# Performance work log

Measured on AMD Instinct MI355X. Metric: run time of the kernel, lower is better.

Reference implementation:

```python
import jax, jax.numpy as jnp
import numpy as np

N_NODES = 100000
N_EDGES = 1600000
IN_C, HID_C, OUT_C = 128, 256, 256


def sage_conv(x, src, dst, W_l, b_l, W_r, n_nodes):
    # mean aggregation of source-node features onto destination nodes
    msg_sum = jax.ops.segment_sum(x[src], dst, num_segments=n_nodes)  # [N, F]
    deg = jax.ops.segment_sum(jnp.ones_like(dst, dtype=x.dtype), dst, num_segments=n_nodes)
    aggr = msg_sum / jnp.maximum(deg, 1.0)[:, None]
    # PyG SAGEConv: lin_l(aggr) (with bias) + lin_r(x) (no bias)
    return aggr @ W_l + b_l + x @ W_r


def setup_inputs() -> dict:
    key = jax.random.key(0)
    ks = jax.random.split(key, 12)
    x = jax.random.normal(ks[0], (N_NODES, IN_C), dtype=jnp.float32)
    edge_src = jax.random.randint(ks[1], (N_EDGES,), 0, N_NODES)
    edge_dst = jax.random.randint(ks[2], (N_EDGES,), 0, N_NODES)

    def glorot(k, fan_in, fan_out):
        s = jnp.sqrt(2.0 / (fan_in + fan_out)).astype(jnp.float32)
        return jax.random.normal(k, (fan_in, fan_out), dtype=jnp.float32) * s

    return {
        "x": x,
        "W_l0": glorot(ks[3], IN_C, HID_C), "b_l0": jnp.zeros((HID_C,), jnp.float32),
        "W_r0": glorot(ks[4], IN_C, HID_C),
        "W_l1": glorot(ks[5], HID_C, HID_C), "b_l1": jnp.zeros((HID_C,), jnp.float32),
        "W_r1": glorot(ks[6], HID_C, HID_C),
        "W_l2": glorot(ks[7], HID_C, OUT_C), "b_l2": jnp.zeros((OUT_C,), jnp.float32),
        "W_r2": glorot(ks[8], HID_C, OUT_C),
        "edge_src": edge_src,
        "edge_dst": edge_dst,
    }


def reference(x, W_l0, b_l0, W_r0, W_l1, b_l1, W_r1, W_l2, b_l2, W_r2, edge_src, edge_dst):
    n = x.shape[0]
    h = sage_conv(x, edge_src, edge_dst, W_l0, b_l0, W_r0, n)
    h = jax.nn.relu(h)  # dropout p=0.0 -> identity
    h = sage_conv(h, edge_src, edge_dst, W_l1, b_l1, W_r1, n)
    h = jax.nn.relu(h)
    h = sage_conv(h, edge_src, edge_dst, W_l2, b_l2, W_r2, n)
    return h
```

## Files before the change

kernel.cpp:

```cpp
#include <hip/hip_runtime.h>
#include <cstdint>
#include <cstddef>


#define N_NODES 100000
#define N_EDGES 1600000

#define SCAN_BLOCKS 256
#define SCAN_T 256
#define FILL_PASSES 4

typedef unsigned short ushort;
typedef unsigned int uint;
typedef __attribute__((ext_vector_type(8))) short short8;
typedef __attribute__((ext_vector_type(4))) float floatx4;

#define AS1 __attribute__((address_space(1)))
#define AS3 __attribute__((address_space(3)))

__device__ __forceinline__ float bf2f(ushort h) {
    union { uint u; float f; } c; c.u = ((uint)h) << 16; return c.f;
}
__device__ __forceinline__ ushort f2bf(float f) {
    union { float f; uint u; } c; c.f = f;
    uint u = c.u;
    return (ushort)((u + 0x7FFFu + ((u >> 16) & 1u)) >> 16);
}


#define N4X (N_NODES * 128 / 4)

__global__ void prep_all(
    const int* __restrict__ dst, int* __restrict__ cnt,
    const float* __restrict__ x, ushort* __restrict__ xb,
    const float* __restrict__ Wl0, ushort* __restrict__ Wl0t,
    const float* __restrict__ Wr0, ushort* __restrict__ Wr0t,
    const float* __restrict__ Wl1, ushort* __restrict__ Wl1t,
    const float* __restrict__ Wr1, ushort* __restrict__ Wr1t,
    const float* __restrict__ Wl2, ushort* __restrict__ Wl2t,
    const float* __restrict__ Wr2, ushort* __restrict__ Wr2t)
{
    int i = blockIdx.x * blockDim.x + threadIdx.x;
    if (i < N_EDGES) { atomicAdd(&cnt[dst[i]], 1); return; }
    i -= N_EDGES;
    if (i < N4X) {
        float4 v = *(const float4*)&x[(size_t)i * 4];
        ushort4 o;
        o.x = f2bf(v.x); o.y = f2bf(v.y); o.z = f2bf(v.z); o.w = f2bf(v.w);
        *(ushort4*)&xb[(size_t)i * 4] = o;
        return;
    }
    i -= N4X;
#define WT2(Wsrc, Wdst, LIM) \
    if (i < (LIM)) { \
        int q = i >> 11, col = (i >> 3) & 255, e = i & 7; \
        Wdst[i] = f2bf(Wsrc[(q * 8 + e) * 256 + col]); \
        return; \
    } \
    i -= (LIM);
    WT2(Wl0, Wl0t, 32768)
    WT2(Wr0, Wr0t, 32768)
    WT2(Wl1, Wl1t, 65536)
    WT2(Wr1, Wr1t, 65536)
    WT2(Wl2, Wl2t, 65536)
    WT2(Wr2, Wr2t, 65536)
#undef WT2
}


__global__ __launch_bounds__(SCAN_T) void scan_partial(
    const int* __restrict__ cnt, int* __restrict__ bsum, int n)
{
    int chunk = (n + SCAN_BLOCKS - 1) / SCAN_BLOCKS;
    int beg = blockIdx.x * chunk;
    int end = beg + chunk; if (end > n) end = n;
    int t = threadIdx.x;
    int s = 0;
    for (int i = beg + t; i < end; i += SCAN_T) s += cnt[i];
    __shared__ int sh[SCAN_T];
    sh[t] = s;
    __syncthreads();
    for (int off = SCAN_T / 2; off > 0; off >>= 1) {
        if (t < off) sh[t] += sh[t + off];
        __syncthreads();
    }
    if (t == 0) bsum[blockIdx.x] = sh[0];
}

__global__ __launch_bounds__(SCAN_T) void scan_block_sums(int* __restrict__ bsum) {
    int t = threadIdx.x;
    __shared__ int sh[SCAN_T];
    int v = bsum[t];
    sh[t] = v;
    __syncthreads();
    for (int off = 1; off < SCAN_T; off <<= 1) {
        int u = (t >= off) ? sh[t - off] : 0;
        __syncthreads();
        sh[t] += u;
        __syncthreads();
    }
    bsum[t] = sh[t] - v;
}

__global__ __launch_bounds__(SCAN_T) void scan_fill(
    int* __restrict__ cnt, const int* __restrict__ bsum,
    int* __restrict__ row_ptr, int n)
{
    int chunk = (n + SCAN_BLOCKS - 1) / SCAN_BLOCKS;
    int beg = blockIdx.x * chunk;
    int end = beg + chunk; if (end > n) end = n;
    int t = threadIdx.x;
    int per = (chunk + SCAN_T - 1) / SCAN_T;
    int tb = beg + t * per;
    int te = tb + per; if (te > end) te = end;
    int s = 0;
    for (int i = tb; i < te; ++i) s += cnt[i];
    __shared__ int sh[SCAN_T];
    sh[t] = s;
    __syncthreads();
    for (int off = 1; off < SCAN_T; off <<= 1) {
        int u = (t >= off) ? sh[t - off] : 0;
        __syncthreads();
        sh[t] += u;
        __syncthreads();
    }
    int running = bsum[blockIdx.x] + sh[t] - s;
    for (int i = tb; i < te; ++i) {
        int c = cnt[i];
        row_ptr[i] = running;
        cnt[i] = running;
        running += c;
    }
    if (blockIdx.x == 0 && t == 0) row_ptr[n] = N_EDGES;
}

__global__ void fill_csr(const int* __restrict__ src, const int* __restrict__ dst,
                         int* __restrict__ cursor, int* __restrict__ col_idx) {
    int i = blockIdx.x * blockDim.x + threadIdx.x;
    if (i >= N_EDGES) return;
    int lo = (int)blockIdx.y * (N_NODES / FILL_PASSES);
    int hi = lo + (N_NODES / FILL_PASSES);
    int d = dst[i];
    if (d >= lo && d < hi) {
        int p = atomicAdd(&cursor[d], 1);
        col_idx[p] = src[i];
    }
}

__global__ __launch_bounds__(64) void aggregate_bf16(
    const ushort* __restrict__ xb, const int* __restrict__ row_ptr,
    const int* __restrict__ col_idx, ushort* __restrict__ outb, int F)
{
    int node = blockIdx.x;
    int t = threadIdx.x;
    int b = row_ptr[node], e = row_ptr[node + 1];
    float d = (float)(e - b); if (d < 1.f) d = 1.f;
    float inv = 1.f / d;

    if (F == 256) {
        int c = t * 4;
        float a0 = 0.f, a1 = 0.f, a2 = 0.f, a3 = 0.f;
        float b0 = 0.f, b1 = 0.f, b2 = 0.f, b3 = 0.f;
        int i = b;
        for (; i + 1 < e; i += 2) {
            int s0 = col_idx[i];
            int s1 = col_idx[i + 1];
            uint2 v0 = *(const uint2*)&xb[(size_t)s0 * 256 + c];
            uint2 v1 = *(const uint2*)&xb[(size_t)s1 * 256 + c];
            a0 += bf2f((ushort)(v0.x & 0xffff)); a1 += bf2f((ushort)(v0.x >> 16));
            a2 += bf2f((ushort)(v0.y & 0xffff)); a3 += bf2f((ushort)(v0.y >> 16));
            b0 += bf2f((ushort)(v1.x & 0xffff)); b1 += bf2f((ushort)(v1.x >> 16));
            b2 += bf2f((ushort)(v1.y & 0xffff)); b3 += bf2f((ushort)(v1.y >> 16));
        }
        if (i < e) {
            int s0 = col_idx[i];
            uint2 v0 = *(const uint2*)&xb[(size_t)s0 * 256 + c];
            a0 += bf2f((ushort)(v0.x & 0xffff)); a1 += bf2f((ushort)(v0.x >> 16));
            a2 += bf2f((ushort)(v0.y & 0xffff)); a3 += bf2f((ushort)(v0.y >> 16));
        }
        ushort4 o;
        o.x = f2bf((a0 + b0) * inv); o.y = f2bf((a1 + b1) * inv);
        o.z = f2bf((a2 + b2) * inv); o.w = f2bf((a3 + b3) * inv);
        *(ushort4*)&outb[(size_t)node * 256 + c] = o;
    } else {
        int c = t * 2;
        float a0 = 0.f, a1 = 0.f, b0 = 0.f, b1 = 0.f;
        int i = b;
        for (; i + 1 < e; i += 2) {
            int s0 = col_idx[i];
            int s1 = col_idx[i + 1];
            uint v0 = *(const uint*)&xb[(size_t)s0 * 128 + c];
            uint v1 = *(const uint*)&xb[(size_t)s1 * 128 + c];
            a0 += bf2f((ushort)(v0 & 0xffff)); a1 += bf2f((ushort)(v0 >> 16));
            b0 += bf2f((ushort)(v1 & 0xffff)); b1 += bf2f((ushort)(v1 >> 16));
        }
        if (i < e) {
            int s0 = col_idx[i];
            uint v0 = *(const uint*)&xb[(size_t)s0 * 128 + c];
            a0 += bf2f((ushort)(v0 & 0xffff)); a1 += bf2f((ushort)(v0 >> 16));
        }
        ushort2 o;
        o.x = f2bf((a0 + b0) * inv); o.y = f2bf((a1 + b1) * inv);
        *(ushort2*)&outb[(size_t)node * 128 + c] = o;
    }
}

__global__ __launch_bounds__(256, 2) void gemm_kc(
    const ushort* __restrict__ A1, const ushort* __restrict__ W1t,
    const ushort* __restrict__ A2, const ushort* __restrict__ W2t,
    const float* __restrict__ bias, ushort* __restrict__ out_bf,
    float* __restrict__ out_f32, int M, int K, int relu)
{
    __shared__ __align__(16) ushort Wl[2][2048 * 8];
    int tid = threadIdx.x;
    int w = tid >> 6, lane = tid & 63;
    int m_ = lane & 15, koq = lane >> 4;
    int row0 = blockIdx.x * 128;
    int nc = K >> 6;

    floatx4 acc[2][16];
#pragma unroll
    for (int i = 0; i < 2; ++i)
#pragma unroll
        for (int f = 0; f < 16; ++f) acc[i][f] = (floatx4){0.f, 0.f, 0.f, 0.f};

    int ra = row0 + w * 32 + m_;      if (ra > M - 1) ra = M - 1;
    int rb = row0 + w * 32 + 16 + m_; if (rb > M - 1) rb = M - 1;

#define STAGE(c, buf) \
    { \
        const ushort* _s = &Wt[(size_t)(c) * 16384 + tid * 8]; \
        _Pragma("unroll") \
        for (int j = 0; j < 8; ++j) { \
            __builtin_amdgcn_global_load_lds( \
                (const AS1 uint*)&_s[(size_t)j * 2048], \
                (AS3 uint*)&Wl[buf][(j * 256 + w * 64) * 8], 16, 0, 0); \
        } \
    }

    for (int mm = 0; mm < 2; ++mm) {
        const ushort* __restrict__ A  = mm ? A2 : A1;
        const ushort* __restrict__ Wt = mm ? W2t : W1t;
        const ushort* __restrict__ Aa = &A[(size_t)ra * K + koq * 8];
        const ushort* __restrict__ Ab = &A[(size_t)rb * K + koq * 8];

        STAGE(0, 0)
        short8 a0 = *(const short8*)&Aa[0];
        short8 a1 = *(const short8*)&Ab[0];
        short8 a2 = *(const short8*)&Aa[32];
        short8 a3 = *(const short8*)&Ab[32];
        __syncthreads();

        for (int c = 0; c < nc; ++c) {
            short8 n0, n1, n2, n3;
            if (c + 1 < nc) {
                STAGE(c + 1, (c + 1) & 1)
                n0 = *(const short8*)&Aa[(c + 1) * 64];
                n1 = *(const short8*)&Ab[(c + 1) * 64];
                n2 = *(const short8*)&Aa[(c + 1) * 64 + 32];
                n3 = *(const short8*)&Ab[(c + 1) * 64 + 32];
            }
            int buf = c & 1;
#pragma unroll
            for (int kk = 0; kk < 2; ++kk) {
                const ushort* bb = &Wl[buf][((kk * 4 + koq) * 256 + m_) * 8];
                short8 aA = kk ? a2 : a0;
                short8 aB = kk ? a3 : a1;
#pragma unroll
                for (int fc = 0; fc < 16; ++fc) {
                    short8 b = *(const short8*)&bb[fc * 128];
                    acc[0][fc] = __builtin_amdgcn_mfma_f32_16x16x32_bf16(aA, b, acc[0][fc], 0, 0, 0);
                    acc[1][fc] = __builtin_amdgcn_mfma_f32_16x16x32_bf16(aB, b, acc[1][fc], 0, 0, 0);
                }
            }
            __syncthreads();
            a0 = n0; a1 = n1; a2 = n2; a3 = n3;
        }
    }
#undef STAGE

#pragma unroll
    for (int m2 = 0; m2 < 2; ++m2) {
#pragma unroll
        for (int fc = 0; fc < 16; ++fc) {
            int col = fc * 16 + m_;
            float bv = bias[col];
#pragma unroll
            for (int r = 0; r < 4; ++r) {
                int row = row0 + w * 32 + m2 * 16 + koq * 4 + r;
                if (row >= M) continue;
                float v = acc[m2][fc][r] + bv;
                if (relu) v = fmaxf(v, 0.f);
                if (out_f32) out_f32[(size_t)row * 256 + col] = v;
                else         out_bf [(size_t)row * 256 + col] = f2bf(v);
            }
        }
    }
}


extern "C" void kernel_launch(void* const* d_in, const int* in_sizes, int n_in,
                              void* d_out, int out_size, void* d_ws, size_t ws_size,
                              hipStream_t stream) {
    const float* x    = (const float*)d_in[0];
    const float* W_l0 = (const float*)d_in[1];
    const float* b_l0 = (const float*)d_in[2];
    const float* W_r0 = (const float*)d_in[3];
    const float* W_l1 = (const float*)d_in[4];
    const float* b_l1 = (const float*)d_in[5];
    const float* W_r1 = (const float*)d_in[6];
    const float* W_l2 = (const float*)d_in[7];
    const float* b_l2 = (const float*)d_in[8];
    const float* W_r2 = (const float*)d_in[9];
    const int* esrc   = (const int*)d_in[10];
    const int* edst   = (const int*)d_in[11];
    float* out = (float*)d_out;

    size_t off = 0;
    char* ws = (char*)d_ws;
    auto take = [&](size_t bytes) -> void* {
        void* p = ws + off;
        off += (bytes + 255) & ~(size_t)255;
        return p;
    };
    int*    cnt     = (int*)take((size_t)N_NODES * 4);
    int*    row_ptr = (int*)take((size_t)(N_NODES + 1) * 4);
    int*    col_idx = (int*)take((size_t)N_EDGES * 4);
    int*    bsum    = (int*)take((size_t)SCAN_BLOCKS * 4);
    ushort* xb      = (ushort*)take((size_t)N_NODES * 128 * 2);
    ushort* Wl0t    = (ushort*)take((size_t)256 * 128 * 2);
    ushort* Wr0t    = (ushort*)take((size_t)256 * 128 * 2);
    ushort* Wl1t    = (ushort*)take((size_t)256 * 256 * 2);
    ushort* Wr1t    = (ushort*)take((size_t)256 * 256 * 2);
    ushort* Wl2t    = (ushort*)take((size_t)256 * 256 * 2);
    ushort* Wr2t    = (ushort*)take((size_t)256 * 256 * 2);
    ushort* aggrb   = (ushort*)take((size_t)N_NODES * 256 * 2);
    ushort* ha      = (ushort*)take((size_t)N_NODES * 256 * 2);
    ushort* hb      = (ushort*)take((size_t)N_NODES * 256 * 2);
    (void)ws_size; (void)in_sizes; (void)n_in; (void)out_size;

    hipMemsetAsync(cnt, 0, (size_t)N_NODES * 4, stream);
    int total_prep = N_EDGES + N4X + 2 * 32768 + 4 * 65536;
    prep_all<<<(total_prep + 255) / 256, 256, 0, stream>>>(
        edst, cnt, x, xb,
        W_l0, Wl0t, W_r0, Wr0t, W_l1, Wl1t, W_r1, Wr1t, W_l2, Wl2t, W_r2, Wr2t);

    scan_partial<<<SCAN_BLOCKS, SCAN_T, 0, stream>>>(cnt, bsum, N_NODES);
    scan_block_sums<<<1, SCAN_T, 0, stream>>>(bsum);
    scan_fill<<<SCAN_BLOCKS, SCAN_T, 0, stream>>>(cnt, bsum, row_ptr, N_NODES);
    int eb = (N_EDGES + 255) / 256;
    fill_csr<<<dim3(eb, FILL_PASSES), 256, 0, stream>>>(esrc, edst, cnt, col_idx);

    dim3 ggrid((N_NODES + 127) / 128, 1);

    aggregate_bf16<<<N_NODES, 64, 0, stream>>>(xb, row_ptr, col_idx, aggrb, 128);
    gemm_kc<<<ggrid, 256, 0, stream>>>(aggrb, Wl0t, xb, Wr0t, b_l0,
                                       ha, nullptr, N_NODES, 128, 1);
    aggregate_bf16<<<N_NODES, 64, 0, stream>>>(ha, row_ptr, col_idx, aggrb, 256);
    gemm_kc<<<ggrid, 256, 0, stream>>>(aggrb, Wl1t, ha, Wr1t, b_l1,
                                       hb, nullptr, N_NODES, 256, 1);
    aggregate_bf16<<<N_NODES, 64, 0, stream>>>(hb, row_ptr, col_idx, aggrb, 256);
    gemm_kc<<<ggrid, 256, 0, stream>>>(aggrb, Wl2t, hb, Wr2t, b_l2,
                                       nullptr, out, N_NODES, 256, 0);
}
```

Measured before the change: 808.9 us.

## Stream GEMM weight fragments from global memory directly into registers, bypassing LDS

Rewrites the fused dual-GEMM kernel so each lane loads its B (weight) fragments straight from global memory into registers every 32-wide k step. The LDS double buffer, the async global-to-LDS staging and the per-chunk block barriers are all removed. The intent is to cut LDS traffic and synchronisation and rely on L2/L1 caching of the small shared weight matrix. In exchange every wave re-reads the weights from the cache hierarchy, load latency is less hidden, and register pressure rises from holding 16 B fragments.

```diff
diff --git a/kernel.cpp b/kernel.cpp
--- a/kernel.cpp
+++ b/kernel.cpp
@@ -205,18 +205,17 @@
     }
 }
 
-__global__ __launch_bounds__(256, 2) void gemm_kc(
+__global__ __launch_bounds__(256, 2) void gemm_stream(
     const ushort* __restrict__ A1, const ushort* __restrict__ W1t,
     const ushort* __restrict__ A2, const ushort* __restrict__ W2t,
     const float* __restrict__ bias, ushort* __restrict__ out_bf,
     float* __restrict__ out_f32, int M, int K, int relu)
 {
-    __shared__ __align__(16) ushort Wl[2][2048 * 8];
     int tid = threadIdx.x;
     int w = tid >> 6, lane = tid & 63;
     int m_ = lane & 15, koq = lane >> 4;
     int row0 = blockIdx.x * 128;
-    int nc = K >> 6;
+    int nk = K >> 5;
 
     floatx4 acc[2][16];
 #pragma unroll
@@ -226,58 +225,42 @@
 
     int ra = row0 + w * 32 + m_;      if (ra > M - 1) ra = M - 1;
     int rb = row0 + w * 32 + 16 + m_; if (rb > M - 1) rb = M - 1;
-
-#define STAGE(c, buf) \
-    { \
-        const ushort* _s = &Wt[(size_t)(c) * 16384 + tid * 8]; \
-        _Pragma("unroll") \
-        for (int j = 0; j < 8; ++j) { \
-            __builtin_amdgcn_global_load_lds( \
-                (const AS1 uint*)&_s[(size_t)j * 2048], \
-                (AS3 uint*)&Wl[buf][(j * 256 + w * 64) * 8], 16, 0, 0); \
-        } \
-    }
 
     for (int mm = 0; mm < 2; ++mm) {
         const ushort* __restrict__ A  = mm ? A2 : A1;
         const ushort* __restrict__ Wt = mm ? W2t : W1t;
         const ushort* __restrict__ Aa = &A[(size_t)ra * K + koq * 8];
         const ushort* __restrict__ Ab = &A[(size_t)rb * K + koq * 8];
-
-        STAGE(0, 0)
+        const ushort* __restrict__ Wb = &Wt[(size_t)((koq << 8) + m_) * 8];
+
         short8 a0 = *(const short8*)&Aa[0];
         short8 a1 = *(const short8*)&Ab[0];
-        short8 a2 = *(const short8*)&Aa[32];
-        short8 a3 = *(const short8*)&Ab[32];
-        __syncthreads();
-
-        for (int c = 0; c < nc; ++c) {
-            short8 n0, n1, n2, n3;
-            if (c + 1 < nc) {
-                STAGE(c + 1, (c + 1) & 1)
-                n0 = *(const short8*)&Aa[(c + 1) * 64];
-                n1 = *(const short8*)&Ab[(c + 1) * 64];
-                n2 = *(const short8*)&Aa[(c + 1) * 64 + 32];
-                n3 = *(const short8*)&Ab[(c + 1) * 64 + 32];
+        for (int g = 0; g < nk; ++g) {
+            short8 b0[8], b1[8];
+#pragma unroll
+            for (int j = 0; j < 8; ++j)
+                b0[j] = *(const short8*)&Wb[(size_t)g * 8192 + j * 128];
+#pragma unroll
+            for (int j = 0; j < 8; ++j)
+                b1[j] = *(const short8*)&Wb[(size_t)g * 8192 + (8 + j) * 128];
+#pragma unroll
+            for (int j = 0; j < 8; ++j) {
+                acc[0][j] = __builtin_amdgcn_mfma_f32_16x16x32_bf16(a0, b0[j], acc[0][j], 0, 0, 0);
+                acc[1][j] = __builtin_amdgcn_mfma_f32_16x16x32_bf16(a1, b0[j], acc[1][j], 0, 0, 0);
             }
-            int buf = c & 1;
-#pragma unroll
-            for (int kk = 0; kk < 2; ++kk) {
-                const ushort* bb = &Wl[buf][((kk * 4 + koq) * 256 + m_) * 8];
-                short8 aA = kk ? a2 : a0;
-                short8 aB = kk ? a3 : a1;
-#pragma unroll
-                for (int fc = 0; fc < 16; ++fc) {
-                    short8 b = *(const short8*)&bb[fc * 128];
-                    acc[0][fc] = __builtin_amdgcn_mfma_f32_16x16x32_bf16(aA, b, acc[0][fc], 0, 0, 0);
-                    acc[1][fc] = __builtin_amdgcn_mfma_f32_16x16x32_bf16(aB, b, acc[1][fc], 0, 0, 0);
-                }
+            short8 n0, n1;
+            if (g + 1 < nk) {
+                n0 = *(const short8*)&Aa[(g + 1) * 32];
+                n1 = *(const short8*)&Ab[(g + 1) * 32];
             }
-            __syncthreads();
-            a0 = n0; a1 = n1; a2 = n2; a3 = n3;
-        }
-    }
-#undef STAGE
+#pragma unroll
+            for (int j = 0; j < 8; ++j) {
+                acc[0][8 + j] = __builtin_amdgcn_mfma_f32_16x16x32_bf16(a0, b1[j], acc[0][8 + j], 0, 0, 0);
+                acc[1][8 + j] = __builtin_amdgcn_mfma_f32_16x16x32_bf16(a1, b1[j], acc[1][8 + j], 0, 0, 0);
+            }
+            a0 = n0; a1 = n1;
+        }
+    }
 
 #pragma unroll
     for (int m2 = 0; m2 < 2; ++m2) {
@@ -354,12 +337,12 @@
     dim3 ggrid((N_NODES + 127) / 128, 1);
 
     aggregate_bf16<<<N_NODES, 64, 0, stream>>>(xb, row_ptr, col_idx, aggrb, 128);
-    gemm_kc<<<ggrid, 256, 0, stream>>>(aggrb, Wl0t, xb, Wr0t, b_l0,
-                                       ha, nullptr, N_NODES, 128, 1);
+    gemm_stream<<<ggrid, 256, 0, stream>>>(aggrb, Wl0t, xb, Wr0t, b_l0,
+                                           ha, nullptr, N_NODES, 128, 1);
     aggregate_bf16<<<N_NODES, 64, 0, stream>>>(ha, row_ptr, col_idx, aggrb, 256);
-    gemm_kc<<<ggrid, 256, 0, stream>>>(aggrb, Wl1t, ha, Wr1t, b_l1,
-                                       hb, nullptr, N_NODES, 256, 1);
+    gemm_stream<<<ggrid, 256, 0, stream>>>(aggrb, Wl1t, ha, Wr1t, b_l1,
+                                           hb, nullptr, N_NODES, 256, 1);
     aggregate_bf16<<<N_NODES, 64, 0, stream>>>(hb, row_ptr, col_idx, aggrb, 256);
-    gemm_kc<<<ggrid, 256, 0, stream>>>(aggrb, Wl2t, hb, Wr2t, b_l2,
-                                       nullptr, out, N_NODES, 256, 0);
-}
+    gemm_stream<<<ggrid, 256, 0, stream>>>(aggrb, Wl2t, hb, Wr2t, b_l2,
+                                           nullptr, out, N_NODES, 256, 0);
+}
```

Measured after the change: 886.6 us. +9.6%, slower.
